# Kernel tuning notes

Hardware: AMD Instinct MI355X
Metric: run time of the kernel (lower is better)

## Reference

```python
import jax, jax.numpy as jnp
import numpy as np

U, D_IN, RANK, N = 128, 10240, 320, 32

def setup_inputs() -> dict:
    key = jax.random.key(0)
    ks = jax.random.split(key, 9)
    s = 0.02
    return {
        "x": jax.random.normal(ks[0], (U, D_IN), jnp.float32),
        "h": jax.random.normal(ks[1], (U, D_IN, N), jnp.float32),
        "W_delta": jax.random.normal(ks[2], (D_IN, RANK), jnp.float32) * s,
        "W_dt": jax.random.normal(ks[3], (RANK, D_IN), jnp.float32) * s,
        "b_dt": jax.random.normal(ks[4], (D_IN,), jnp.float32) * s,
        "W_B": jax.random.normal(ks[5], (D_IN, N), jnp.float32) * s,
        "W_C": jax.random.normal(ks[6], (D_IN, N), jnp.float32) * s,
        # A = -exp(A_log): strictly negative, so exp(delta*A) in (0,1)
        "A": -jnp.exp(jax.random.normal(ks[7], (D_IN, N), jnp.float32) * 0.5),
        "D": jax.random.normal(ks[8], (D_IN,), jnp.float32),
    }

def reference(x, h, W_delta, W_dt, b_dt, W_B, W_C, A, D):
    # dt projection: low-rank then up-proj + bias, softplus (beta=1, threshold=20)
    delta = jax.nn.softplus(x @ W_delta @ W_dt + b_dt)          # [U, D_IN]
    # B and C input-dependent projections
    B = x @ W_B                                                  # [U, N]
    C = x @ W_C                                                  # [U, N]
    # discretize: abar = exp(delta * A); bbar*x = delta * B * x
    abar = jnp.exp(delta[:, :, None] * A[None, :, :])            # [U, D_IN, N]
    bx = (delta * x)[:, :, None] * B[:, None, :]                 # [U, D_IN, N]
    h_new = abar * h + bx                                        # state update
    # output: y_d = sum_n h[d,n] * C[n] + D_d * x_d
    y = jnp.einsum('udn,un->ud', h_new, C) + D[None, :] * x      # [U, D_IN]
    return y, h_new
```

## Files before the change

### kernel.cpp

```cpp
#include <hip/hip_runtime.h>

#define U_    128
#define DIN   10240
#define RANK  320
#define NS    32

__global__ __launch_bounds__(64) void proj_kernel(
    const float* __restrict__ x,
    const float* __restrict__ Wd, const float* __restrict__ Wb,
    const float* __restrict__ Wc,
    float* __restrict__ t_out, float* __restrict__ B_out, float* __restrict__ C_out)
{
    int b = blockIdx.x;
    const float* W; float* out; int ldw, ncols, n0, u0, k0;
    if (b < 800) {
        int nt = b % 5; int ut = (b / 5) % 8; int kc = b / 40;
        W = Wd; out = t_out; ldw = RANK; ncols = RANK;
        n0 = nt * 64; u0 = ut * 16; k0 = kc * 512;
    } else if (b < 960) {
        int b2 = b - 800; int ut = b2 % 8; int kc = b2 / 8;
        W = Wb; out = B_out; ldw = NS; ncols = NS;
        n0 = 0; u0 = ut * 16; k0 = kc * 512;
    } else {
        int b2 = b - 960; int ut = b2 % 8; int kc = b2 / 8;
        W = Wc; out = C_out; ldw = NS; ncols = NS;
        n0 = 0; u0 = ut * 16; k0 = kc * 512;
    }
    int lane = threadIdx.x;
    int n = n0 + lane;
    bool valid = (n < ncols);
    int ns = valid ? n : 0;

    float acc[16];
#pragma unroll
    for (int i = 0; i < 16; ++i) acc[i] = 0.f;

    const float* xrow = x + (size_t)u0 * DIN;
#pragma unroll 4
    for (int k = k0; k < k0 + 512; ++k) {
        float w = valid ? W[(size_t)k * ldw + ns] : 0.f;
#pragma unroll
        for (int i = 0; i < 16; ++i)
            acc[i] += xrow[(size_t)i * DIN + k] * w;
    }
    if (valid) {
#pragma unroll
        for (int i = 0; i < 16; ++i)
            atomicAdd(&out[(size_t)(u0 + i) * ldw + n], acc[i]);
    }
}

__global__ __launch_bounds__(64) void delta_kernel(
    const float* __restrict__ t, const float* __restrict__ Wdt,
    const float* __restrict__ b_dt, float* __restrict__ delta)
{
    int b = blockIdx.x;
    int dt_ = b % 160; int ut = b / 160;
    int d = dt_ * 64 + threadIdx.x;
    int u0 = ut * 16;

    float bias = b_dt[d];
    float acc[16];
#pragma unroll
    for (int i = 0; i < 16; ++i) acc[i] = bias;

    const float* trow = t + (size_t)u0 * RANK;
#pragma unroll 4
    for (int r = 0; r < RANK; ++r) {
        float w = Wdt[(size_t)r * DIN + d];
#pragma unroll
        for (int i = 0; i < 16; ++i)
            acc[i] += trow[(size_t)i * RANK + r] * w;
    }
#pragma unroll
    for (int i = 0; i < 16; ++i) {
        float z = acc[i];
        float sp = (z > 20.f) ? z : log1pf(__expf(z));
        delta[(size_t)(u0 + i) * DIN + d] = sp;
    }
}

__global__ __launch_bounds__(256) void ssm_kernel(
    const float* __restrict__ x, const float* __restrict__ h,
    const float* __restrict__ delta,
    const float* __restrict__ Bc, const float* __restrict__ Cc,
    const float* __restrict__ A, const float* __restrict__ Dvec,
    float* __restrict__ y, float* __restrict__ hnew)
{
    int idx4 = blockIdx.x * 256 + threadIdx.x;
    int n4 = idx4 & 7;
    int ud = idx4 >> 3;
    int d = ud % DIN;
    int u = ud / DIN;

    float dlt = delta[ud];
    float xv  = x[ud];

    float4 hv = ((const float4*)h)[idx4];
    float4 av = ((const float4*)A)[(size_t)d * 8 + n4];
    float4 bv = ((const float4*)Bc)[u * 8 + n4];
    float4 cv = ((const float4*)Cc)[u * 8 + n4];

    float dx = dlt * xv;
    float4 hn;
    hn.x = __expf(dlt * av.x) * hv.x + dx * bv.x;
    hn.y = __expf(dlt * av.y) * hv.y + dx * bv.y;
    hn.z = __expf(dlt * av.z) * hv.z + dx * bv.z;
    hn.w = __expf(dlt * av.w) * hv.w + dx * bv.w;

    ((float4*)hnew)[idx4] = hn;

    float p = hn.x * cv.x + hn.y * cv.y + hn.z * cv.z + hn.w * cv.w;
    p += __shfl_xor(p, 4, 8);
    p += __shfl_xor(p, 2, 8);
    p += __shfl_xor(p, 1, 8);
    if (n4 == 0)
        y[ud] = p + Dvec[d] * xv;
}

extern "C" void kernel_launch(void* const* d_in, const int* in_sizes, int n_in,
                              void* d_out, int out_size, void* d_ws, size_t ws_size,
                              hipStream_t stream)
{
    const float* x   = (const float*)d_in[0];
    const float* h   = (const float*)d_in[1];
    const float* Wd  = (const float*)d_in[2];
    const float* Wdt = (const float*)d_in[3];
    const float* bdt = (const float*)d_in[4];
    const float* Wb  = (const float*)d_in[5];
    const float* Wc  = (const float*)d_in[6];
    const float* A   = (const float*)d_in[7];
    const float* Dv  = (const float*)d_in[8];

    float* ws    = (float*)d_ws;
    float* t     = ws;
    float* Bc    = ws + 40960;
    float* Cc    = ws + 45056;
    float* delta = ws + 49152;

    float* y    = (float*)d_out;
    float* hnew = y + (size_t)U_ * DIN;

    hipMemsetAsync(d_ws, 0, 49152 * sizeof(float), stream);

    proj_kernel <<<1120, 64, 0, stream>>>(x, Wd, Wb, Wc, t, Bc, Cc);
    delta_kernel<<<1280, 64, 0, stream>>>(t, Wdt, bdt, delta);
    ssm_kernel  <<<40960, 256, 0, stream>>>(x, h, delta, Bc, Cc, A, Dv, y, hnew);
}
```

Before: 484.4 us.

## Transpose x and use split-K partial buffers with a reduction instead of atomics

Adds a transpose of x so the projection GEMM reads contiguous per-user columns. The x@[W_delta|W_B|W_C] GEMM is restructured so each thread owns one user and 32 output columns. K-chunk partials are written to a buffer and summed by a separate reduce kernel, replacing the atomics and the memset. The delta kernel now reads a transposed t with broadcast loads and processes 32 users per block. The cost is two extra launches and extra workspace traffic for the transpose and the partials.

New measurement: 481.7 us. No clear change (-0.5%).

```diff
diff --git a/kernel.cpp b/kernel.cpp
--- a/kernel.cpp
+++ b/kernel.cpp
@@ -4,76 +4,104 @@
 #define DIN   10240
 #define RANK  320
 #define NS    32
+#define NTOT  384
+#define KC    32
+#define KCH   (DIN / KC)
 
-__global__ __launch_bounds__(64) void proj_kernel(
-    const float* __restrict__ x,
+__global__ __launch_bounds__(256) void transpose_kernel(
+    const float* __restrict__ x, float* __restrict__ xT)
+{
+    __shared__ float tile[32][33];
+    int kb = blockIdx.x * 32, ub = blockIdx.y * 32;
+    int tx = threadIdx.x, ty = threadIdx.y;
+#pragma unroll
+    for (int i = 0; i < 32; i += 8)
+        tile[ty + i][tx] = x[(size_t)(ub + ty + i) * DIN + kb + tx];
+    __syncthreads();
+#pragma unroll
+    for (int i = 0; i < 32; i += 8)
+        xT[(size_t)(kb + ty + i) * U_ + ub + tx] = tile[tx][ty + i];
+}
+
+__global__ __launch_bounds__(64) void gemmA_kernel(
+    const float* __restrict__ xT,
     const float* __restrict__ Wd, const float* __restrict__ Wb,
     const float* __restrict__ Wc,
-    float* __restrict__ t_out, float* __restrict__ B_out, float* __restrict__ C_out)
+    float* __restrict__ partial)
 {
-    int b = blockIdx.x;
-    const float* W; float* out; int ldw, ncols, n0, u0, k0;
-    if (b < 800) {
-        int nt = b % 5; int ut = (b / 5) % 8; int kc = b / 40;
-        W = Wd; out = t_out; ldw = RANK; ncols = RANK;
-        n0 = nt * 64; u0 = ut * 16; k0 = kc * 512;
-    } else if (b < 960) {
-        int b2 = b - 800; int ut = b2 % 8; int kc = b2 / 8;
-        W = Wb; out = B_out; ldw = NS; ncols = NS;
-        n0 = 0; u0 = ut * 16; k0 = kc * 512;
-    } else {
-        int b2 = b - 960; int ut = b2 % 8; int kc = b2 / 8;
-        W = Wc; out = C_out; ldw = NS; ncols = NS;
-        n0 = 0; u0 = ut * 16; k0 = kc * 512;
+    int b  = blockIdx.x;
+    int uh = b & 1;
+    int nt = (b >> 1) % 12;
+    int kc = b / 24;
+    int u  = uh * 64 + threadIdx.x;
+    int n0 = nt * 32;
+
+    const float* W; int ldw, c0;
+    if (nt < 10)       { W = Wd; ldw = RANK; c0 = n0; }
+    else if (nt == 10) { W = Wb; ldw = NS;   c0 = 0;  }
+    else               { W = Wc; ldw = NS;   c0 = 0;  }
+
+    float acc[32];
+#pragma unroll
+    for (int j = 0; j < 32; ++j) acc[j] = 0.f;
+
+    int k0 = kc * KCH;
+    const float* Wp = W  + (size_t)k0 * ldw + c0;
+    const float* xp = xT + (size_t)k0 * U_ + u;
+
+#pragma unroll 2
+    for (int k = 0; k < KCH; ++k) {
+        float xv = xp[(size_t)k * U_];
+#pragma unroll
+        for (int j = 0; j < 32; ++j)
+            acc[j] += xv * Wp[(size_t)k * ldw + j];
     }
-    int lane = threadIdx.x;
-    int n = n0 + lane;
-    bool valid = (n < ncols);
-    int ns = valid ? n : 0;
 
-    float acc[16];
+    float* out = partial + (size_t)kc * (NTOT * U_) + (size_t)n0 * U_ + u;
 #pragma unroll
-    for (int i = 0; i < 16; ++i) acc[i] = 0.f;
+    for (int j = 0; j < 32; ++j)
+        out[(size_t)j * U_] = acc[j];
+}
 
-    const float* xrow = x + (size_t)u0 * DIN;
-#pragma unroll 4
-    for (int k = k0; k < k0 + 512; ++k) {
-        float w = valid ? W[(size_t)k * ldw + ns] : 0.f;
-#pragma unroll
-        for (int i = 0; i < 16; ++i)
-            acc[i] += xrow[(size_t)i * DIN + k] * w;
-    }
-    if (valid) {
-#pragma unroll
-        for (int i = 0; i < 16; ++i)
-            atomicAdd(&out[(size_t)(u0 + i) * ldw + n], acc[i]);
-    }
+__global__ __launch_bounds__(256) void reduce_kernel(
+    const float* __restrict__ partial, float* __restrict__ tT,
+    float* __restrict__ Bc, float* __restrict__ Cc)
+{
+    int e = blockIdx.x * 256 + threadIdx.x;
+    float s = 0.f;
+#pragma unroll 8
+    for (int kc = 0; kc < KC; ++kc)
+        s += partial[(size_t)kc * (NTOT * U_) + e];
+    int n = e >> 7, u = e & 127;
+    if (n < RANK)            tT[e] = s;
+    else if (n < RANK + NS)  Bc[u * NS + (n - RANK)] = s;
+    else                     Cc[u * NS + (n - RANK - NS)] = s;
 }
 
 __global__ __launch_bounds__(64) void delta_kernel(
-    const float* __restrict__ t, const float* __restrict__ Wdt,
+    const float* __restrict__ tT, const float* __restrict__ Wdt,
     const float* __restrict__ b_dt, float* __restrict__ delta)
 {
-    int b = blockIdx.x;
-    int dt_ = b % 160; int ut = b / 160;
-    int d = dt_ * 64 + threadIdx.x;
-    int u0 = ut * 16;
+    int b  = blockIdx.x;
+    int dt_ = b % 160, ut = b / 160;
+    int d  = dt_ * 64 + threadIdx.x;
+    int u0 = ut * 32;
 
     float bias = b_dt[d];
-    float acc[16];
+    float acc[32];
 #pragma unroll
-    for (int i = 0; i < 16; ++i) acc[i] = bias;
+    for (int i = 0; i < 32; ++i) acc[i] = bias;
 
-    const float* trow = t + (size_t)u0 * RANK;
-#pragma unroll 4
+#pragma unroll 2
     for (int r = 0; r < RANK; ++r) {
         float w = Wdt[(size_t)r * DIN + d];
+        const float* tp = tT + r * U_ + u0;
 #pragma unroll
-        for (int i = 0; i < 16; ++i)
-            acc[i] += trow[(size_t)i * RANK + r] * w;
+        for (int i = 0; i < 32; ++i)
+            acc[i] += w * tp[i];
     }
 #pragma unroll
-    for (int i = 0; i < 16; ++i) {
+    for (int i = 0; i < 32; ++i) {
         float z = acc[i];
         float sp = (z > 20.f) ? z : log1pf(__expf(z));
         delta[(size_t)(u0 + i) * DIN + d] = sp;
@@ -132,18 +160,21 @@
     const float* A   = (const float*)d_in[7];
     const float* Dv  = (const float*)d_in[8];
 
-    float* ws    = (float*)d_ws;
-    float* t     = ws;
-    float* Bc    = ws + 40960;
-    float* Cc    = ws + 45056;
-    float* delta = ws + 49152;
+    float* ws      = (float*)d_ws;
+    float* xT      = ws;
+    float* partial = ws + 1310720;
+    float* delta   = partial;
+    float* tT      = ws + 1310720 + 1572864;
+    float* Bc      = tT + 40960;
+    float* Cc      = Bc + 4096;
 
     float* y    = (float*)d_out;
     float* hnew = y + (size_t)U_ * DIN;
 
-    hipMemsetAsync(d_ws, 0, 49152 * sizeof(float), stream);
-
-    proj_kernel <<<1120, 64, 0, stream>>>(x, Wd, Wb, Wc, t, Bc, Cc);
-    delta_kernel<<<1280, 64, 0, stream>>>(t, Wdt, bdt, delta);
-    ssm_kernel  <<<40960, 256, 0, stream>>>(x, h, delta, Bc, Cc, A, Dv, y, hnew);
+    dim3 tb(32, 8);
+    transpose_kernel<<<dim3(DIN / 32, U_ / 32), tb, 0, stream>>>(x, xT);
+    gemmA_kernel    <<<768, 64, 0, stream>>>(xT, Wd, Wb, Wc, partial);
+    reduce_kernel   <<<192, 256, 0, stream>>>(partial, tT, Bc, Cc);
+    delta_kernel    <<<640, 64, 0, stream>>>(tT, Wdt, bdt, delta);
+    ssm_kernel      <<<40960, 256, 0, stream>>>(x, h, delta, Bc, Cc, A, Dv, y, hnew);
 }
```
